# Kernel tuning notes

Measured on AMD Instinct MI355X. Metric: run time of the kernel, lower is better.

The kernel has to match this reference:

```python
import jax, jax.numpy as jnp
import numpy as np

N_SRC, N_TGT, E, L, C_OUT = 100000, 200000, 500000, 256, 2


def setup_inputs() -> dict:
    key = jax.random.key(0)
    ks = jax.random.split(key, 10)
    s = 1.0 / np.sqrt(L)
    return {
        "pos_source": jax.random.normal(ks[0], (N_SRC, 3), jnp.float32),
        "pos_target": jax.random.normal(ks[1], (N_TGT, 3), jnp.float32),
        "latents": jax.random.normal(ks[2], (N_SRC, L), jnp.float32),
        "row": jax.random.randint(ks[3], (E,), 0, N_TGT),
        "col": jax.random.randint(ks[4], (E,), 0, N_SRC),
        "W_in": jax.random.normal(ks[5], (L + 3, L), jnp.float32) * s,
        "b_in": jnp.zeros((L,), jnp.float32),
        "W1": jax.random.normal(ks[6], (L, L), jnp.float32) * s,
        "b1": jnp.zeros((L,), jnp.float32),
        "W2": jax.random.normal(ks[7], (L, L), jnp.float32) * s,
        "b2": jnp.zeros((L,), jnp.float32),
        "W_out": jax.random.normal(ks[8], (L, C_OUT), jnp.float32) * s,
        "b_out": jnp.zeros((C_OUT,), jnp.float32),
    }


def reference(pos_source, pos_target, latents, row, col,
              W_in, b_in, W1, b1, W2, b2, W_out, b_out):
    # gather relative positions and latents per neighbor pair: [E, 3], [E, L]
    pos_rel = pos_target[row] - pos_source[col]
    x = jnp.concatenate([latents[col], pos_rel], axis=1)  # [E, L+3]
    x = x @ W_in + b_in                                   # fc_in
    x = jax.nn.relu(x) @ W1 + b1                          # mlp layer 0 (act first)
    x = jax.nn.relu(x) @ W2 + b2                          # mlp layer 1
    x = x @ W_out + b_out                                 # fc_out (no activation)
    return x[:, 0]                                        # predictions
```

## Files before the change

kernel.cpp:

```cpp
#include <hip/hip_runtime.h>
#include <hip/hip_bf16.h>
#include <stdint.h>

typedef __attribute__((ext_vector_type(8))) short bf16x8;
typedef __attribute__((ext_vector_type(4))) float f32x4;

#define NSRC 100000
#define WIN_OFF 0
#define W1P_OFF (128*1024)
#define BU_OFF  (256*1024)
#define SS_OFF  (BU_OFF + 2048)
#define Y_OFF   (264*1024)

#define PAIRB 1040
#define XBYTES (32*PAIRB)
#define POFF(r) (((r)>>1)*PAIRB + ((r)&1)*512)

#define AS3U32(p) ((__attribute__((address_space(3))) uint32_t*)(uintptr_t)(p))
#define AS1U32(p) ((const __attribute__((address_space(1))) uint32_t*)(uintptr_t)(p))

__global__ __launch_bounds__(256) void pack_kernel(
    const float* __restrict__ Win, const float* __restrict__ W1,
    const float* __restrict__ W2, const float* __restrict__ Wout,
    const float* __restrict__ b1, const float* __restrict__ b2,
    const float* __restrict__ b_out, char* __restrict__ wp)
{
    const int t = threadIdx.x, blk = blockIdx.x;
    if (blk < 16) {
        const float* W = (blk < 8) ? Win : W1;
        char* dst = wp + ((blk < 8) ? WIN_OFF : W1P_OFF);
        const int c = blk & 7;
        #pragma unroll
        for (int q = 0; q < 4; ++q) {
            union { bf16x8 v; __hip_bfloat16 h[8]; } u;
            #pragma unroll
            for (int j = 0; j < 8; ++j)
                u.h[j] = __float2bfloat16(W[(size_t)(c*32 + q*8 + j)*256 + t]);
            *(bf16x8*)(dst + c*16384 + t*64 + q*16) = u.v;
        }
    } else if (blk < 24) {
        __shared__ float w0s[256];
        w0s[t] = Wout[t*2];
        __syncthreads();
        const int b = blk - 16, fl = t >> 3, sub = t & 7, f = b*32 + fl;
        const float* row = W2 + (size_t)f*256 + sub*32;
        float p = 0.f;
        #pragma unroll
        for (int j = 0; j < 32; ++j) p += row[j]*w0s[sub*32 + j];
        p += __shfl_xor(p,1); p += __shfl_xor(p,2); p += __shfl_xor(p,4);
        if (sub == 0) {
            float2 v; v.x = b1[f]; v.y = p;
            *(float2*)(wp + BU_OFF + f*8) = v;
        }
    } else {
        __shared__ float rb[4];
        float v = b2[t]*Wout[t*2];
        v += __shfl_xor(v,1); v += __shfl_xor(v,2); v += __shfl_xor(v,4);
        v += __shfl_xor(v,8); v += __shfl_xor(v,16); v += __shfl_xor(v,32);
        if ((t&63) == 0) rb[t>>6] = v;
        __syncthreads();
        if (t == 0) *(float*)(wp + SS_OFF) = rb[0]+rb[1]+rb[2]+rb[3] + b_out[0];
    }
}

__global__ __launch_bounds__(256, 2) void precompute_y(
    const float* __restrict__ latents, const float* __restrict__ b_in,
    const char* __restrict__ wp, char* __restrict__ Yc)
{
    __shared__ __align__(16) char Xs[XBYTES];
    __shared__ float binS[256];
    const int tid = threadIdx.x, wave = tid >> 6, lane = tid & 63;
    const int q = lane >> 4, lm = lane & 15;

    bf16x8 wA[4][8];
    {
        const char* wb = wp + WIN_OFF;
        #pragma unroll
        for (int mt = 0; mt < 4; ++mt) {
            const int m = wave*64 + mt*16 + lm;
            #pragma unroll
            for (int c = 0; c < 8; ++c)
                wA[mt][c] = *(const bf16x8*)(wb + c*16384 + m*64 + q*16);
        }
    }
    binS[tid] = b_in[tid];

    const int ntY = (NSRC + 63) / 64;
    for (int tile = blockIdx.x; tile < ntY; tile += 512) {
        const int base = tile*64;
        {
            const int r = tid & 63, h = tid >> 6;
            int srow = base + r; if (srow >= NSRC) srow = NSRC - 1;
            const float4* lp = (const float4*)(latents + (size_t)srow*256 + h*64);
            #pragma unroll
            for (int w = 0; w < 8; ++w) {
                float4 v0 = lp[w*2], v1 = lp[w*2+1];
                union { bf16x8 v; __hip_bfloat16 hh[8]; } u;
                u.hh[0]=__float2bfloat16(v0.x); u.hh[1]=__float2bfloat16(v0.y);
                u.hh[2]=__float2bfloat16(v0.z); u.hh[3]=__float2bfloat16(v0.w);
                u.hh[4]=__float2bfloat16(v1.x); u.hh[5]=__float2bfloat16(v1.y);
                u.hh[6]=__float2bfloat16(v1.z); u.hh[7]=__float2bfloat16(v1.w);
                *(bf16x8*)(Xs + POFF(r) + h*128 + w*16) = u.v;
            }
        }
        __syncthreads();
        f32x4 acc[4][4];
        #pragma unroll
        for (int mt = 0; mt < 4; ++mt)
            #pragma unroll
            for (int nt = 0; nt < 4; ++nt) acc[mt][nt] = (f32x4){0.f,0.f,0.f,0.f};
        #pragma unroll
        for (int c = 0; c < 8; ++c) {
            bf16x8 b[4];
            #pragma unroll
            for (int nt = 0; nt < 4; ++nt)
                b[nt] = *(const bf16x8*)(Xs + POFF(nt*16+lm) + c*64 + q*16);
            #pragma unroll
            for (int mt = 0; mt < 4; ++mt)
                #pragma unroll
                for (int nt = 0; nt < 4; ++nt)
                    acc[mt][nt] = __builtin_amdgcn_mfma_f32_16x16x32_bf16(wA[mt][c], b[nt], acc[mt][nt], 0,0,0);
        }
        #pragma unroll
        for (int mt = 0; mt < 4; ++mt) {
            const int f0 = wave*64 + mt*16 + q*4;
            float4 bb = *(const float4*)&binS[f0];
            float bbv[4] = {bb.x, bb.y, bb.z, bb.w};
            #pragma unroll
            for (int nt = 0; nt < 4; ++nt) {
                const int srow = base + nt*16 + lm;
                if (srow < NSRC) {
                    union { uint2 uu; __hip_bfloat16 hh[4]; } pk;
                    #pragma unroll
                    for (int rg = 0; rg < 4; ++rg)
                        pk.hh[rg] = __float2bfloat16(acc[mt][nt][rg] + bbv[rg]);
                    *(uint2*)(Yc + (size_t)srow*512 + f0*2) = pk.uu;
                }
            }
        }
        __syncthreads();
    }
}

__global__ __launch_bounds__(256, 2) void interp_main(
    const float* __restrict__ pos_src, const float* __restrict__ pos_tgt,
    const int* __restrict__ rowi, const int* __restrict__ coli,
    const float* __restrict__ Win, const char* __restrict__ wp,
    const char* __restrict__ Yc, float* __restrict__ out,
    int E, int ntiles)
{
    __shared__ __align__(16) char Xs[2][XBYTES];
    __shared__ float wposI[32][24];
    __shared__ float buS[512];
    __shared__ float posrel[2][64][4];
    __shared__ int   colsS[2][64];
    __shared__ float red[4][64];

    const int tid = threadIdx.x, wave = tid >> 6, lane = tid & 63;
    const int q = lane >> 4, lm = lane & 15;
    const int bid = blockIdx.x;

    bf16x8 wA[4][8];
    {
        const char* wb = wp + W1P_OFF;
        #pragma unroll
        for (int mt = 0; mt < 4; ++mt) {
            const int m = wave*64 + mt*16 + lm;
            #pragma unroll
            for (int c = 0; c < 8; ++c)
                wA[mt][c] = *(const bf16x8*)(wb + c*16384 + m*64 + q*16);
        }
    }
    {
        #pragma unroll
        for (int s = 0; s < 3; ++s)
            wposI[tid >> 3][s*8 + (tid & 7)] = Win[(size_t)(256+s)*256 + tid];
        *(float2*)&buS[tid*2] = *(const float2*)(wp + BU_OFF + tid*8);
    }
    const float Sv = *(const float*)(wp + SS_OFF);
    const int niter = (ntiles - bid + 511) / 512;

    #pragma unroll
    for (int ii = 0; ii < 2; ++ii) {
        if (tid < 64) {
            long tt = (long)bid + (long)ii*512; if (tt >= ntiles) tt = ntiles - 1;
            long e = tt*64 + tid; if (e >= E) e = E - 1;
            int ri = rowi[e], ci = coli[e];
            colsS[ii][tid] = ci;
            float4 pr;
            pr.x = pos_tgt[ri*3+0] - pos_src[ci*3+0];
            pr.y = pos_tgt[ri*3+1] - pos_src[ci*3+1];
            pr.z = pos_tgt[ri*3+2] - pos_src[ci*3+2];
            pr.w = 0.f;
            *(float4*)&posrel[ii][tid][0] = pr;
        }
    }
    __syncthreads();
    {
        #pragma unroll
        for (int k2 = 0; k2 < 8; ++k2) {
            const int r0 = wave*16 + k2*2;
            const int row = r0 + (lane >> 5);
            const int cv = colsS[0][row];
            const char* src = Yc + (size_t)cv*512 + (lane & 31)*16;
            __builtin_amdgcn_global_load_lds(AS1U32(src), AS3U32(Xs[0] + (r0>>1)*PAIRB), 16, 0, 0);
        }
    }

    for (int i = 0; i < niter; ++i) {
        const int p = i & 1;
        __syncthreads();

        if (i > 0 && tid < 64) {
            long e = ((long)bid + (long)(i-1)*512)*64 + tid;
            if (e < E) out[e] = red[0][tid]+red[1][tid]+red[2][tid]+red[3][tid] + Sv;
        }
        int m_ci = 0; float4 m_pr = {0.f,0.f,0.f,0.f};
        if (tid < 64) {
            long tt = (long)bid + (long)(i+2)*512; if (tt >= ntiles) tt = ntiles - 1;
            long e = tt*64 + tid; if (e >= E) e = E - 1;
            int ri = rowi[e]; m_ci = coli[e];
            m_pr.x = pos_tgt[ri*3+0] - pos_src[m_ci*3+0];
            m_pr.y = pos_tgt[ri*3+1] - pos_src[m_ci*3+1];
            m_pr.z = pos_tgt[ri*3+2] - pos_src[m_ci*3+2];
        }
        {
            const int fs = tid & 31, rb = tid >> 5;
            float w0v[8], w1v[8], w2v[8];
            {
                const float* wi = &wposI[fs][0];
                #pragma unroll
                for (int j = 0; j < 8; ++j) { w0v[j]=wi[j]; w1v[j]=wi[8+j]; w2v[j]=wi[16+j]; }
            }
            char* xb = Xs[p];
            #pragma unroll
            for (int ii2 = 0; ii2 < 8; ++ii2) {
                const int r = rb*8 + ii2;
                float4 pr = *(const float4*)&posrel[p][r][0];
                char* addr = xb + POFF(r) + fs*16;
                union { bf16x8 v; __hip_bfloat16 h[8]; } u;
                u.v = *(bf16x8*)addr;
                #pragma unroll
                for (int j = 0; j < 8; ++j) {
                    float vv = __bfloat162float(u.h[j]) + pr.x*w0v[j] + pr.y*w1v[j] + pr.z*w2v[j];
                    u.h[j] = __float2bfloat16(vv < 0.f ? 0.f : vv);
                }
                *(bf16x8*)addr = u.v;
            }
        }
        __syncthreads();

        {
            const int s = 1 - p;
            char* xb = Xs[s];
            #pragma unroll
            for (int k2 = 0; k2 < 8; ++k2) {
                const int r0 = wave*16 + k2*2;
                const int row = r0 + (lane >> 5);
                const int cv = colsS[s][row];
                const char* src = Yc + (size_t)cv*512 + (lane & 31)*16;
                __builtin_amdgcn_global_load_lds(AS1U32(src), AS3U32(xb + (r0>>1)*PAIRB), 16, 0, 0);
            }
        }
        f32x4 acc[4][4];
        #pragma unroll
        for (int mt = 0; mt < 4; ++mt)
            #pragma unroll
            for (int nt = 0; nt < 4; ++nt) acc[mt][nt] = (f32x4){0.f,0.f,0.f,0.f};
        {
            const char* xb = Xs[p];
            #pragma unroll
            for (int c = 0; c < 8; ++c) {
                bf16x8 b[4];
                #pragma unroll
                for (int nt = 0; nt < 4; ++nt)
                    b[nt] = *(const bf16x8*)(xb + POFF(nt*16+lm) + c*64 + q*16);
                #pragma unroll
                for (int mt = 0; mt < 4; ++mt)
                    #pragma unroll
                    for (int nt = 0; nt < 4; ++nt)
                        acc[mt][nt] = __builtin_amdgcn_mfma_f32_16x16x32_bf16(wA[mt][c], b[nt], acc[mt][nt], 0,0,0);
            }
        }
        float partial[4] = {0.f,0.f,0.f,0.f};
        #pragma unroll
        for (int mt = 0; mt < 4; ++mt) {
            const int f0 = wave*64 + mt*16 + q*4;
            float4 bu0 = *(const float4*)&buS[f0*2];
            float4 bu1 = *(const float4*)&buS[f0*2 + 4];
            float b1v[4] = {bu0.x, bu0.z, bu1.x, bu1.z};
            float uv[4]  = {bu0.y, bu0.w, bu1.y, bu1.w};
            #pragma unroll
            for (int nt = 0; nt < 4; ++nt)
                #pragma unroll
                for (int rg = 0; rg < 4; ++rg) {
                    float h = acc[mt][nt][rg] + b1v[rg];
                    if (h > 0.f) partial[nt] += h * uv[rg];
                }
        }
        #pragma unroll
        for (int nt = 0; nt < 4; ++nt) {
            float v = partial[nt];
            v += __shfl_xor(v, 16);
            v += __shfl_xor(v, 32);
            if (lane < 16) red[wave][nt*16 + lane] = v;
        }
        if (tid < 64) {
            colsS[p][tid] = m_ci;
            *(float4*)&posrel[p][tid][0] = m_pr;
        }
    }
    __syncthreads();
    if (tid < 64) {
        long e = ((long)bid + (long)(niter-1)*512)*64 + tid;
        if (e < E) out[e] = red[0][tid]+red[1][tid]+red[2][tid]+red[3][tid] + Sv;
    }
}

extern "C" void kernel_launch(void* const* d_in, const int* in_sizes, int n_in,
                              void* d_out, int out_size, void* d_ws, size_t ws_size,
                              hipStream_t stream)
{
    const float* pos_src = (const float*)d_in[0];
    const float* pos_tgt = (const float*)d_in[1];
    const float* latents = (const float*)d_in[2];
    const int*   rowi    = (const int*)d_in[3];
    const int*   coli    = (const int*)d_in[4];
    const float* Win     = (const float*)d_in[5];
    const float* b_in    = (const float*)d_in[6];
    const float* W1      = (const float*)d_in[7];
    const float* b1      = (const float*)d_in[8];
    const float* W2      = (const float*)d_in[9];
    const float* b2      = (const float*)d_in[10];
    const float* Wout    = (const float*)d_in[11];
    const float* b_out   = (const float*)d_in[12];
    float* out = (float*)d_out;
    const int E = in_sizes[3];
    const int ntiles = (E + 63) / 64;

    char* wp = (char*)d_ws;
    char* Yc = wp + Y_OFF;

    pack_kernel<<<25, 256, 0, stream>>>(Win, W1, W2, Wout, b1, b2, b_out, wp);
    precompute_y<<<512, 256, 0, stream>>>(latents, b_in, wp, Yc);
    interp_main<<<512, 256, 0, stream>>>(pos_src, pos_tgt, rowi, coli,
                                         Win, wp, Yc, out, E, ntiles);
}
```

Baseline: 310.3 us.

## Bucket-sort edges by source column to improve Y-gather locality

Adds a counting sort of edges by col>>4 (histogram, single-block scan, atomic scatter to a permutation). The main kernel then processes edges in permuted order, gathering the precomputed Y rows for nearby source nodes together, and scatters outputs back through the permutation. The aim is better L2 locality for the 512-byte-per-edge Y gathers. The cost is three extra kernel launches, atomics, indirect index loads and scattered output writes. The new path is only taken when the workspace is large enough.

```diff
diff --git a/kernel.cpp b/kernel.cpp
--- a/kernel.cpp
+++ b/kernel.cpp
@@ -11,6 +11,10 @@
 #define BU_OFF  (256*1024)
 #define SS_OFF  (BU_OFF + 2048)
 #define Y_OFF   (264*1024)
+#define SORT_OFF (Y_OFF + (size_t)NSRC*512)
+
+#define SHIFT 4
+#define NBUCK ((NSRC + (1<<SHIFT) - 1) >> SHIFT)
 
 #define PAIRB 1040
 #define XBYTES (32*PAIRB)
@@ -23,7 +27,8 @@
     const float* __restrict__ Win, const float* __restrict__ W1,
     const float* __restrict__ W2, const float* __restrict__ Wout,
     const float* __restrict__ b1, const float* __restrict__ b2,
-    const float* __restrict__ b_out, char* __restrict__ wp)
+    const float* __restrict__ b_out, char* __restrict__ wp,
+    int* __restrict__ hist)
 {
     const int t = threadIdx.x, blk = blockIdx.x;
     if (blk < 16) {
@@ -52,7 +57,7 @@
             float2 v; v.x = b1[f]; v.y = p;
             *(float2*)(wp + BU_OFF + f*8) = v;
         }
-    } else {
+    } else if (blk == 24) {
         __shared__ float rb[4];
         float v = b2[t]*Wout[t*2];
         v += __shfl_xor(v,1); v += __shfl_xor(v,2); v += __shfl_xor(v,4);
@@ -60,6 +65,58 @@
         if ((t&63) == 0) rb[t>>6] = v;
         __syncthreads();
         if (t == 0) *(float*)(wp + SS_OFF) = rb[0]+rb[1]+rb[2]+rb[3] + b_out[0];
+    } else {
+        const int idx = (blk - 25)*256 + t;
+        if (idx < NBUCK) hist[idx] = 0;
+    }
+}
+
+__global__ __launch_bounds__(256) void hist_kernel(
+    const int* __restrict__ coli, int* __restrict__ hist, int E)
+{
+    int i = blockIdx.x*256 + threadIdx.x;
+    for (; i < E; i += gridDim.x*256)
+        atomicAdd(&hist[coli[i] >> SHIFT], 1);
+}
+
+__global__ __launch_bounds__(1024) void scan_kernel(
+    const int* __restrict__ hist, int* __restrict__ off)
+{
+    __shared__ int part[1024];
+    const int t = threadIdx.x;
+    const int base = t * 7;
+    int v[7]; int s = 0;
+    #pragma unroll
+    for (int j = 0; j < 7; ++j) {
+        const int idx = base + j;
+        int h = (idx < NBUCK) ? hist[idx] : 0;
+        v[j] = s; s += h;
+    }
+    part[t] = s;
+    __syncthreads();
+    for (int d = 1; d < 1024; d <<= 1) {
+        int x = (t >= d) ? part[t - d] : 0;
+        __syncthreads();
+        part[t] += x;
+        __syncthreads();
+    }
+    const int pre = (t == 0) ? 0 : part[t - 1];
+    #pragma unroll
+    for (int j = 0; j < 7; ++j) {
+        const int idx = base + j;
+        if (idx < NBUCK) off[idx] = pre + v[j];
+    }
+}
+
+__global__ __launch_bounds__(256) void scatter_kernel(
+    const int* __restrict__ coli, int* __restrict__ off,
+    int* __restrict__ perm, int E)
+{
+    int i = blockIdx.x*256 + threadIdx.x;
+    for (; i < E; i += gridDim.x*256) {
+        const int c = coli[i];
+        const int p = atomicAdd(&off[c >> SHIFT], 1);
+        perm[p] = i;
     }
 }
 
@@ -145,6 +202,7 @@
 __global__ __launch_bounds__(256, 2) void interp_main(
     const float* __restrict__ pos_src, const float* __restrict__ pos_tgt,
     const int* __restrict__ rowi, const int* __restrict__ coli,
+    const int* __restrict__ perm,
     const float* __restrict__ Win, const char* __restrict__ wp,
     const char* __restrict__ Yc, float* __restrict__ out,
     int E, int ntiles)
@@ -179,13 +237,15 @@
     }
     const float Sv = *(const float*)(wp + SS_OFF);
     const int niter = (ntiles - bid + 511) / 512;
+    int pe = 0;
 
     #pragma unroll
     for (int ii = 0; ii < 2; ++ii) {
         if (tid < 64) {
             long tt = (long)bid + (long)ii*512; if (tt >= ntiles) tt = ntiles - 1;
             long e = tt*64 + tid; if (e >= E) e = E - 1;
-            int ri = rowi[e], ci = coli[e];
+            const int pidx = perm ? perm[e] : (int)e;
+            int ri = rowi[pidx], ci = coli[pidx];
             colsS[ii][tid] = ci;
             float4 pr;
             pr.x = pos_tgt[ri*3+0] - pos_src[ci*3+0];
@@ -211,15 +271,20 @@
         const int p = i & 1;
         __syncthreads();
 
-        if (i > 0 && tid < 64) {
-            long e = ((long)bid + (long)(i-1)*512)*64 + tid;
-            if (e < E) out[e] = red[0][tid]+red[1][tid]+red[2][tid]+red[3][tid] + Sv;
+        if (tid < 64) {
+            if (i > 0) {
+                long e = ((long)bid + (long)(i-1)*512)*64 + tid;
+                if (e < E) out[pe] = red[0][tid]+red[1][tid]+red[2][tid]+red[3][tid] + Sv;
+            }
+            long ec = ((long)bid + (long)i*512)*64 + tid;
+            if (ec < E) pe = perm ? perm[ec] : (int)ec;
         }
         int m_ci = 0; float4 m_pr = {0.f,0.f,0.f,0.f};
         if (tid < 64) {
             long tt = (long)bid + (long)(i+2)*512; if (tt >= ntiles) tt = ntiles - 1;
             long e = tt*64 + tid; if (e >= E) e = E - 1;
-            int ri = rowi[e]; m_ci = coli[e];
+            const int pidx = perm ? perm[e] : (int)e;
+            int ri = rowi[pidx]; m_ci = coli[pidx];
             m_pr.x = pos_tgt[ri*3+0] - pos_src[m_ci*3+0];
             m_pr.y = pos_tgt[ri*3+1] - pos_src[m_ci*3+1];
             m_pr.z = pos_tgt[ri*3+2] - pos_src[m_ci*3+2];
@@ -313,7 +378,7 @@
     __syncthreads();
     if (tid < 64) {
         long e = ((long)bid + (long)(niter-1)*512)*64 + tid;
-        if (e < E) out[e] = red[0][tid]+red[1][tid]+red[2][tid]+red[3][tid] + Sv;
+        if (e < E) out[pe] = red[0][tid]+red[1][tid]+red[2][tid]+red[3][tid] + Sv;
     }
 }
 
@@ -341,8 +406,21 @@
     char* wp = (char*)d_ws;
     char* Yc = wp + Y_OFF;
 
-    pack_kernel<<<25, 256, 0, stream>>>(Win, W1, W2, Wout, b1, b2, b_out, wp);
+    const size_t sort_need = SORT_OFF + 2*32*1024 + (size_t)E*4;
+    const bool use_sort = (ws_size >= sort_need);
+    int* hist = (int*)(wp + SORT_OFF);
+    int* off  = hist + 8192;
+    int* perm = off + 8192;
+
+    pack_kernel<<<use_sort ? 50 : 25, 256, 0, stream>>>(
+        Win, W1, W2, Wout, b1, b2, b_out, wp, hist);
+    if (use_sort) {
+        hist_kernel<<<512, 256, 0, stream>>>(coli, hist, E);
+        scan_kernel<<<1, 1024, 0, stream>>>(hist, off);
+        scatter_kernel<<<512, 256, 0, stream>>>(coli, off, perm, E);
+    }
     precompute_y<<<512, 256, 0, stream>>>(latents, b_in, wp, Yc);
     interp_main<<<512, 256, 0, stream>>>(pos_src, pos_tgt, rowi, coli,
+                                         use_sort ? perm : (const int*)nullptr,
                                          Win, wp, Yc, out, E, ntiles);
 }
```

New measurement: 411.6 us. 32.6% more time.

## Double-buffer latent tiles via async global-to-LDS loads in precompute_y

Applied to the files above, without the earlier changes.

Rewrites the source-node projection kernel to stage 32-row fp32 latent tiles straight into LDS with global_load_lds, double-buffered so the next tile's load overlaps the current tile's MFMA work. Conversion to bf16 now happens when fragments are read from LDS, not when tiles are stored, and tile height drops from 64 to 32 rows. This is meant to hide global load latency and cut register pressure, at the cost of more LDS per block, more LDS read traffic, and more loop iterations. It assumes NSRC is divisible by 32 and drops the tail guard.

```diff
diff --git a/kernel.cpp b/kernel.cpp
--- a/kernel.cpp
+++ b/kernel.cpp
@@ -15,6 +15,8 @@
 #define PAIRB 1040
 #define XBYTES (32*PAIRB)
 #define POFF(r) (((r)>>1)*PAIRB + ((r)&1)*512)
+
+#define L32 1040
 
 #define AS3U32(p) ((__attribute__((address_space(3))) uint32_t*)(uintptr_t)(p))
 #define AS1U32(p) ((const __attribute__((address_space(1))) uint32_t*)(uintptr_t)(p))
@@ -67,7 +69,7 @@
     const float* __restrict__ latents, const float* __restrict__ b_in,
     const char* __restrict__ wp, char* __restrict__ Yc)
 {
-    __shared__ __align__(16) char Xs[XBYTES];
+    __shared__ __align__(16) char Ls[2][32*L32];
     __shared__ float binS[256];
     const int tid = threadIdx.x, wave = tid >> 6, lane = tid & 63;
     const int q = lane >> 4, lm = lane & 15;
@@ -85,40 +87,55 @@
     }
     binS[tid] = b_in[tid];
 
-    const int ntY = (NSRC + 63) / 64;
-    for (int tile = blockIdx.x; tile < ntY; tile += 512) {
-        const int base = tile*64;
-        {
-            const int r = tid & 63, h = tid >> 6;
-            int srow = base + r; if (srow >= NSRC) srow = NSRC - 1;
-            const float4* lp = (const float4*)(latents + (size_t)srow*256 + h*64);
-            #pragma unroll
-            for (int w = 0; w < 8; ++w) {
-                float4 v0 = lp[w*2], v1 = lp[w*2+1];
-                union { bf16x8 v; __hip_bfloat16 hh[8]; } u;
-                u.hh[0]=__float2bfloat16(v0.x); u.hh[1]=__float2bfloat16(v0.y);
-                u.hh[2]=__float2bfloat16(v0.z); u.hh[3]=__float2bfloat16(v0.w);
-                u.hh[4]=__float2bfloat16(v1.x); u.hh[5]=__float2bfloat16(v1.y);
-                u.hh[6]=__float2bfloat16(v1.z); u.hh[7]=__float2bfloat16(v1.w);
-                *(bf16x8*)(Xs + POFF(r) + h*128 + w*16) = u.v;
-            }
-        }
-        __syncthreads();
-        f32x4 acc[4][4];
+    const int nt32 = NSRC / 32;
+    const int t0 = blockIdx.x;
+
+    #define STAGE32(t, buf) do {                                               \
+        const float* __lat = latents + (size_t)(t)*32*256;                     \
+        _Pragma("unroll")                                                      \
+        for (int j = 0; j < 8; ++j) {                                          \
+            const int r = wave*8 + j;                                          \
+            __builtin_amdgcn_global_load_lds(                                  \
+                AS1U32((const char*)(__lat + (size_t)r*256) + lane*16),        \
+                AS3U32((buf) + r*L32), 16, 0, 0);                              \
+        }                                                                      \
+    } while (0)
+
+    if (t0 < nt32) STAGE32(t0, Ls[0]);
+
+    int it = 0;
+    for (int t = t0; t < nt32; t += 512, ++it) {
+        const int p = it & 1;
+        __syncthreads();
+        if (t + 512 < nt32) STAGE32(t + 512, Ls[1 - p]);
+
+        f32x4 acc[4][2];
         #pragma unroll
         for (int mt = 0; mt < 4; ++mt)
             #pragma unroll
-            for (int nt = 0; nt < 4; ++nt) acc[mt][nt] = (f32x4){0.f,0.f,0.f,0.f};
+            for (int nt = 0; nt < 2; ++nt) acc[mt][nt] = (f32x4){0.f,0.f,0.f,0.f};
+
+        const char* lb = Ls[p];
         #pragma unroll
         for (int c = 0; c < 8; ++c) {
-            bf16x8 b[4];
-            #pragma unroll
-            for (int nt = 0; nt < 4; ++nt)
-                b[nt] = *(const bf16x8*)(Xs + POFF(nt*16+lm) + c*64 + q*16);
+            bf16x8 b[2];
+            #pragma unroll
+            for (int nt = 0; nt < 2; ++nt) {
+                const int n = nt*16 + lm;
+                const float* fp = (const float*)(lb + n*L32 + c*128 + q*32);
+                float4 f0 = *(const float4*)fp;
+                float4 f1 = *(const float4*)(fp + 4);
+                union { bf16x8 v; __hip_bfloat16 h[8]; } u;
+                u.h[0]=__float2bfloat16(f0.x); u.h[1]=__float2bfloat16(f0.y);
+                u.h[2]=__float2bfloat16(f0.z); u.h[3]=__float2bfloat16(f0.w);
+                u.h[4]=__float2bfloat16(f1.x); u.h[5]=__float2bfloat16(f1.y);
+                u.h[6]=__float2bfloat16(f1.z); u.h[7]=__float2bfloat16(f1.w);
+                b[nt] = u.v;
+            }
             #pragma unroll
             for (int mt = 0; mt < 4; ++mt)
                 #pragma unroll
-                for (int nt = 0; nt < 4; ++nt)
+                for (int nt = 0; nt < 2; ++nt)
                     acc[mt][nt] = __builtin_amdgcn_mfma_f32_16x16x32_bf16(wA[mt][c], b[nt], acc[mt][nt], 0,0,0);
         }
         #pragma unroll
@@ -127,19 +144,17 @@
             float4 bb = *(const float4*)&binS[f0];
             float bbv[4] = {bb.x, bb.y, bb.z, bb.w};
             #pragma unroll
-            for (int nt = 0; nt < 4; ++nt) {
-                const int srow = base + nt*16 + lm;
-                if (srow < NSRC) {
-                    union { uint2 uu; __hip_bfloat16 hh[4]; } pk;
-                    #pragma unroll
-                    for (int rg = 0; rg < 4; ++rg)
-                        pk.hh[rg] = __float2bfloat16(acc[mt][nt][rg] + bbv[rg]);
-                    *(uint2*)(Yc + (size_t)srow*512 + f0*2) = pk.uu;
-                }
-            }
-        }
-        __syncthreads();
-    }
+            for (int nt = 0; nt < 2; ++nt) {
+                const int srow = t*32 + nt*16 + lm;
+                union { uint2 uu; __hip_bfloat16 hh[4]; } pk;
+                #pragma unroll
+                for (int rg = 0; rg < 4; ++rg)
+                    pk.hh[rg] = __float2bfloat16(acc[mt][nt][rg] + bbv[rg]);
+                *(uint2*)(Yc + (size_t)srow*512 + f0*2) = pk.uu;
+            }
+        }
+    }
+    #undef STAGE32
 }
 
 __global__ __launch_bounds__(256, 2) void interp_main(
```

Result: no change. 304.5 us (-1.9%).
